# Kernel optimization log

Hardware: AMD Instinct MI355X
Metric: run time of the kernel (lower is better)

Reference implementation:

```python
import jax, jax.numpy as jnp
import numpy as np

N = 50000
E = 800000
F_IN = 128
HID = 32
HEADS = 4
SLOPE = 0.2


def setup_inputs() -> dict:
    key = jax.random.key(0)
    ks = jax.random.split(key, 12)
    x = jax.random.normal(ks[0], (N, F_IN), dtype=jnp.float32)
    edge_index = jax.random.randint(ks[1], (2, E), 0, N, dtype=jnp.int64)
    edge_attr = jax.random.normal(ks[2], (E, 4), dtype=jnp.float32)
    s1 = 1.0 / np.sqrt(F_IN)
    s2 = 1.0 / np.sqrt(HID)
    W1 = jax.random.normal(ks[3], (F_IN, HEADS * HID), dtype=jnp.float32) * s1
    a_src1 = jax.random.normal(ks[4], (HEADS, HID), dtype=jnp.float32) * s2
    a_dst1 = jax.random.normal(ks[5], (HEADS, HID), dtype=jnp.float32) * s2
    b1 = jnp.zeros((HID,), dtype=jnp.float32)
    W2 = jax.random.normal(ks[6], (HID, 1), dtype=jnp.float32) * s2
    a_src2 = jax.random.normal(ks[7], (1, 1), dtype=jnp.float32)
    a_dst2 = jax.random.normal(ks[8], (1, 1), dtype=jnp.float32)
    b2 = jnp.zeros((1,), dtype=jnp.float32)
    return {"input_tensor": x, "edge_index": edge_index, "edge_attr": edge_attr,
            "W1": W1, "a_src1": a_src1, "a_dst1": a_dst1, "b1": b1,
            "W2": W2, "a_src2": a_src2, "a_dst2": a_dst2, "b2": b2}


def _gat_conv(x, src, dst, W, a_src, a_dst, b, heads, out_ch):
    n = x.shape[0]
    h = (x @ W).reshape(n, heads, out_ch)          # [N, H, C]
    alpha_src = jnp.sum(h * a_src, axis=-1)        # [N, H]
    alpha_dst = jnp.sum(h * a_dst, axis=-1)        # [N, H]
    e = alpha_src[src] + alpha_dst[dst]            # [E, H]
    e = jax.nn.leaky_relu(e, negative_slope=SLOPE)
    # segment softmax over edges grouped by destination node
    e_max = jax.ops.segment_max(e, dst, num_segments=n)
    e = jnp.exp(e - e_max[dst])
    denom = jax.ops.segment_sum(e, dst, num_segments=n)
    alpha = e / denom[dst]                         # [E, H]
    msg = h[src] * alpha[..., None]                # [E, H, C]
    out = jax.ops.segment_sum(msg, dst, num_segments=n)  # [N, H, C]
    return out.mean(axis=1) + b                    # concat=False -> mean over heads


def reference(input_tensor, edge_index, edge_attr, W1, a_src1, a_dst1, b1, W2, a_src2, a_dst2, b2):
    # PyG GATConv adds self-loops by default; edge_attr unused (edge_dim=None)
    loops = jnp.arange(N, dtype=edge_index.dtype)
    src = jnp.concatenate([edge_index[0], loops])
    dst = jnp.concatenate([edge_index[1], loops])
    x = _gat_conv(input_tensor, src, dst, W1, a_src1, a_dst1, b1, HEADS, HID)
    x = jax.nn.elu(x)
    x = _gat_conv(x, src, dst, W2, a_src2, a_dst2, b2, 1, 1)
    return x
```

## Files before the change

kernel.cpp:

```cpp
#include <hip/hip_runtime.h>
#include <hip/hip_fp16.h>
#include <math.h>
#include <stdint.h>

static constexpr int kN     = 50000;
static constexpr int kFIn   = 128;
static constexpr int kHeads = 4;
static constexpr int kScanB = 256;
static constexpr int kScanNB = (kN + kScanB - 1) / kScanB;

typedef _Float16 half8v  __attribute__((ext_vector_type(8)));
typedef float    floatx4 __attribute__((ext_vector_type(4)));

__device__ __forceinline__ float lrelu(float x) { return x > 0.f ? x : 0.2f * x; }

__device__ __forceinline__ float pack2h(float a, float b) {
    const __half2 h = __floats2half2_rn(a, b);
    return __uint_as_float(__builtin_bit_cast(uint32_t, h));
}

__global__ void k_init(int* __restrict__ p, int n) {
    int i = blockIdx.x * blockDim.x + threadIdx.x;
    if (i < n) p[i] = 0;
}

__global__ __launch_bounds__(256)
void k_gemm1(const float* __restrict__ x, const float* __restrict__ W1,
             __half* __restrict__ h1h, int nPass, int grid) {
    __shared__ __align__(16) float whf[128 * 16 * 4];
    __shared__ __align__(16) float xsf[32 * 16 * 4];
    const int t = threadIdx.x;
    const int l = t & 63;
    const int g = t >> 6;
    for (int idx = t; idx < 2048; idx += 256) {
        const int c = idx >> 7, col = idx & 127;
        float4 st;
        st.x = pack2h(W1[(8 * c + 0) * 128 + col], W1[(8 * c + 1) * 128 + col]);
        st.y = pack2h(W1[(8 * c + 2) * 128 + col], W1[(8 * c + 3) * 128 + col]);
        st.z = pack2h(W1[(8 * c + 4) * 128 + col], W1[(8 * c + 5) * 128 + col]);
        st.w = pack2h(W1[(8 * c + 6) * 128 + col], W1[(8 * c + 7) * 128 + col]);
        const int gran = col * 16 + ((c + col) & 15);
        *reinterpret_cast<float4*>(&whf[gran * 4]) = st;
    }
    __syncthreads();

    const int rt  = g & 1;
    const int ctB = (g >> 1) * 4;
    const int lm  = l & 15;
    const int lk  = l >> 4;

    for (int pass = blockIdx.x; pass < nPass; pass += grid) {
        const int nodeBase = pass * 32;
        for (int q = t; q < 512; q += 256) {
            const int nn = q >> 4, ck = q & 15;
            int n = nodeBase + nn; if (n >= kN) n = kN - 1;
            const float4 xa = *reinterpret_cast<const float4*>(&x[(size_t)n * 128 + ck * 8]);
            const float4 xb = *reinterpret_cast<const float4*>(&x[(size_t)n * 128 + ck * 8 + 4]);
            float4 st;
            st.x = pack2h(xa.x, xa.y);
            st.y = pack2h(xa.z, xa.w);
            st.z = pack2h(xb.x, xb.y);
            st.w = pack2h(xb.z, xb.w);
            const int gran = nn * 16 + ((ck + nn) & 15);
            *reinterpret_cast<float4*>(&xsf[gran * 4]) = st;
        }
        __syncthreads();

        floatx4 acc0 = {0.f, 0.f, 0.f, 0.f};
        floatx4 acc1 = {0.f, 0.f, 0.f, 0.f};
        floatx4 acc2 = {0.f, 0.f, 0.f, 0.f};
        floatx4 acc3 = {0.f, 0.f, 0.f, 0.f};
        const int node = rt * 16 + lm;
        const int ch0  = ctB * 16 + lm;
#pragma unroll
        for (int kk = 0; kk < 4; ++kk) {
            const int ck = lk + 4 * kk;
            const half8v af = *reinterpret_cast<const half8v*>(
                &xsf[(node * 16 + ((ck + node) & 15)) * 4]);
            const half8v b0 = *reinterpret_cast<const half8v*>(
                &whf[((ch0 +  0) * 16 + ((ck + ch0 +  0) & 15)) * 4]);
            const half8v b1 = *reinterpret_cast<const half8v*>(
                &whf[((ch0 + 16) * 16 + ((ck + ch0 + 16) & 15)) * 4]);
            const half8v b2 = *reinterpret_cast<const half8v*>(
                &whf[((ch0 + 32) * 16 + ((ck + ch0 + 32) & 15)) * 4]);
            const half8v b3 = *reinterpret_cast<const half8v*>(
                &whf[((ch0 + 48) * 16 + ((ck + ch0 + 48) & 15)) * 4]);
            acc0 = __builtin_amdgcn_mfma_f32_16x16x32_f16(af, b0, acc0, 0, 0, 0);
            acc1 = __builtin_amdgcn_mfma_f32_16x16x32_f16(af, b1, acc1, 0, 0, 0);
            acc2 = __builtin_amdgcn_mfma_f32_16x16x32_f16(af, b2, acc2, 0, 0, 0);
            acc3 = __builtin_amdgcn_mfma_f32_16x16x32_f16(af, b3, acc3, 0, 0, 0);
        }
        const int nrow0 = nodeBase + rt * 16 + lk * 4;
#pragma unroll
        for (int r = 0; r < 4; ++r) {
            const int n = nrow0 + r;
            if (n < kN) {
                h1h[(size_t)n * 128 + ch0     ] = __float2half(acc0[r]);
                h1h[(size_t)n * 128 + ch0 + 16] = __float2half(acc1[r]);
                h1h[(size_t)n * 128 + ch0 + 32] = __float2half(acc2[r]);
                h1h[(size_t)n * 128 + ch0 + 48] = __float2half(acc3[r]);
            }
        }
        __syncthreads();
    }
}

__global__ __launch_bounds__(256)
void k_logits(const __half* __restrict__ h1h,
              const float* __restrict__ a_src1, const float* __restrict__ a_dst1,
              float* __restrict__ asrc, float* __restrict__ adst) {
    const int n = blockIdx.x * 4 + (threadIdx.x >> 6);
    if (n >= kN) return;
    const int j = threadIdx.x & 63;
    const float2 f = __half22float2(*(const __half2*)&h1h[(size_t)n * 128 + 2 * j]);
    float ps = f.x * a_src1[2 * j] + f.y * a_src1[2 * j + 1];
    float pd = f.x * a_dst1[2 * j] + f.y * a_dst1[2 * j + 1];
#pragma unroll
    for (int off = 8; off >= 1; off >>= 1) {
        ps += __shfl_xor(ps, off, 64);
        pd += __shfl_xor(pd, off, 64);
    }
    if ((j & 15) == 0) {
        asrc[n * 4 + (j >> 4)] = ps;
        adst[n * 4 + (j >> 4)] = pd;
    }
}

__global__ void k_hist(const int* __restrict__ ei, int E, int* __restrict__ deg,
                       int* __restrict__ rank) {
    int i = blockIdx.x * blockDim.x + threadIdx.x;
    int total = E + kN;
    if (i >= total) return;
    int d = (i < E) ? ei[E + i] : (i - E);
    rank[i] = atomicAdd(&deg[d], 1);
}

__global__ void k_scan_a(const int* __restrict__ deg, int* __restrict__ loc, int* __restrict__ bsum) {
    __shared__ int tmp[kScanB];
    int t = threadIdx.x;
    int i = blockIdx.x * kScanB + t;
    int v = (i < kN) ? deg[i] : 0;
    tmp[t] = v;
    __syncthreads();
    for (int off = 1; off < kScanB; off <<= 1) {
        int add = (t >= off) ? tmp[t - off] : 0;
        __syncthreads();
        tmp[t] += add;
        __syncthreads();
    }
    if (i < kN) loc[i] = tmp[t] - v;
    if (t == kScanB - 1) bsum[blockIdx.x] = tmp[t];
}

__global__ void k_scan_b(int* __restrict__ bsum) {
    __shared__ int tmp[256];
    int t = threadIdx.x;
    int v = (t < kScanNB) ? bsum[t] : 0;
    tmp[t] = v;
    __syncthreads();
    for (int off = 1; off < 256; off <<= 1) {
        int add = (t >= off) ? tmp[t - off] : 0;
        __syncthreads();
        tmp[t] += add;
        __syncthreads();
    }
    if (t < kScanNB) bsum[t] = tmp[t] - v;
}

__global__ void k_scan_c(const int* __restrict__ loc, const int* __restrict__ bsum,
                         int* __restrict__ rowptr, int E2) {
    int i = blockIdx.x * kScanB + threadIdx.x;
    if (i < kN) rowptr[i] = loc[i] + bsum[blockIdx.x];
    if (i == 0) rowptr[kN] = E2;
}

__global__ void k_scatter(const int* __restrict__ ei, int E,
                          const int* __restrict__ rowptr, const int* __restrict__ rank,
                          int* __restrict__ es) {
    int i = blockIdx.x * blockDim.x + threadIdx.x;
    int total = E + kN;
    if (i >= total) return;
    int s, d;
    if (i < E) { s = ei[i]; d = ei[E + i]; } else { s = d = i - E; }
    es[rowptr[d] + rank[i]] = s;
}

__global__ __launch_bounds__(256)
void k_wgt(const int* __restrict__ rowptr, const int* __restrict__ es,
           const float* __restrict__ asrc, const float* __restrict__ adst,
           float* __restrict__ wgt) {
    const int n = blockIdx.x * 16 + (threadIdx.x >> 4);
    if (n >= kN) return;
    const int l = threadIdx.x & 15;
    const int beg = rowptr[n], end = rowptr[n + 1];
    const float ad0 = adst[n * 4 + 0], ad1 = adst[n * 4 + 1];
    const float ad2 = adst[n * 4 + 2], ad3 = adst[n * 4 + 3];
    for (int p = beg + l; p < end; p += 16) {
        const int s = es[p];
        float4 w4;
        w4.x = expf(lrelu(asrc[s * 4 + 0] + ad0));
        w4.y = expf(lrelu(asrc[s * 4 + 1] + ad1));
        w4.z = expf(lrelu(asrc[s * 4 + 2] + ad2));
        w4.w = expf(lrelu(asrc[s * 4 + 3] + ad3));
        *reinterpret_cast<float4*>(&wgt[(size_t)p * 4]) = w4;
    }
}

__global__ __launch_bounds__(256)
void k_agg1(const int* __restrict__ rowptr, const int* __restrict__ es,
            const float* __restrict__ wgt,
            const __half* __restrict__ h1h, const float* __restrict__ b1,
            const float* __restrict__ W2, float* __restrict__ h2) {
    const int n = blockIdx.x * 4 + (threadIdx.x >> 6);
    if (n >= kN) return;
    const int j  = threadIdx.x & 63;
    const int hh = j >> 4;
    const int beg = rowptr[n], end = rowptr[n + 1];
    float ax0 = 0.f, ay0 = 0.f, dn0 = 0.f;
    float ax1 = 0.f, ay1 = 0.f, dn1 = 0.f;
    int p = beg;
    for (; p + 4 <= end; p += 4) {
        const int s0 = es[p],     s1 = es[p + 1];
        const int s2 = es[p + 2], s3 = es[p + 3];
        const float w0 = wgt[(p + 0) * 4 + hh];
        const float w1 = wgt[(p + 1) * 4 + hh];
        const float w2 = wgt[(p + 2) * 4 + hh];
        const float w3 = wgt[(p + 3) * 4 + hh];
        const float2 f0 = __half22float2(*(const __half2*)&h1h[s0 * 128 + 2 * j]);
        const float2 f1 = __half22float2(*(const __half2*)&h1h[s1 * 128 + 2 * j]);
        const float2 f2 = __half22float2(*(const __half2*)&h1h[s2 * 128 + 2 * j]);
        const float2 f3 = __half22float2(*(const __half2*)&h1h[s3 * 128 + 2 * j]);
        ax0 += w0 * f0.x; ay0 += w0 * f0.y; dn0 += w0;
        ax1 += w1 * f1.x; ay1 += w1 * f1.y; dn1 += w1;
        ax0 += w2 * f2.x; ay0 += w2 * f2.y; dn0 += w2;
        ax1 += w3 * f3.x; ay1 += w3 * f3.y; dn1 += w3;
    }
    for (; p < end; ++p) {
        const int s0 = es[p];
        const float w0 = wgt[p * 4 + hh];
        const float2 f0 = __half22float2(*(const __half2*)&h1h[s0 * 128 + 2 * j]);
        ax0 += w0 * f0.x; ay0 += w0 * f0.y; dn0 += w0;
    }
    const float den = dn0 + dn1;
    float vx = (ax0 + ax1) / den;
    float vy = (ay0 + ay1) / den;
    vx += __shfl_xor(vx, 32, 64); vy += __shfl_xor(vy, 32, 64);
    vx += __shfl_xor(vx, 16, 64); vy += __shfl_xor(vy, 16, 64);
    const int m = j & 15;
    float u0 = 0.25f * vx + b1[2 * m];
    float u1 = 0.25f * vy + b1[2 * m + 1];
    u0 = u0 > 0.f ? u0 : expf(u0) - 1.f;
    u1 = u1 > 0.f ? u1 : expf(u1) - 1.f;
    float tsum = u0 * W2[2 * m] + u1 * W2[2 * m + 1];
    tsum += __shfl_xor(tsum, 8, 64);
    tsum += __shfl_xor(tsum, 4, 64);
    tsum += __shfl_xor(tsum, 2, 64);
    tsum += __shfl_xor(tsum, 1, 64);
    if (j == 0) h2[n] = tsum;
}

__global__ __launch_bounds__(256)
void k_agg2(const int* __restrict__ rowptr, const int* __restrict__ es,
            const float* __restrict__ h2,
            const float* __restrict__ a_s2, const float* __restrict__ a_d2,
            const float* __restrict__ b2, float* __restrict__ out) {
    const int n = blockIdx.x * 16 + (threadIdx.x >> 4);
    if (n >= kN) return;
    const int l = threadIdx.x & 15;
    const float as = a_s2[0], ad = a_d2[0];
    const int beg = rowptr[n], end = rowptr[n + 1];
    const float hd = h2[n] * ad;
    float sw = 0.f, swh = 0.f;
    for (int p = beg + l; p < end; p += 16) {
        float hs = h2[es[p]];
        float w = expf(lrelu(hs * as + hd));
        sw += w;
        swh += w * hs;
    }
#pragma unroll
    for (int off = 8; off >= 1; off >>= 1) {
        sw  += __shfl_xor(sw, off, 64);
        swh += __shfl_xor(swh, off, 64);
    }
    if (l == 0) out[n] = swh / sw + b2[0];
}

extern "C" void kernel_launch(void* const* d_in, const int* in_sizes, int n_in,
                              void* d_out, int out_size, void* d_ws, size_t ws_size,
                              hipStream_t stream) {
    const float* x      = (const float*)d_in[0];
    const int*   ei     = (const int*)d_in[1];
    const float* W1     = (const float*)d_in[3];
    const float* a_src1 = (const float*)d_in[4];
    const float* a_dst1 = (const float*)d_in[5];
    const float* b1     = (const float*)d_in[6];
    const float* W2     = (const float*)d_in[7];
    const float* a_src2 = (const float*)d_in[8];
    const float* a_dst2 = (const float*)d_in[9];
    const float* b2     = (const float*)d_in[10];
    float* out = (float*)d_out;

    const int E  = in_sizes[1] / 2;
    const int E2 = E + kN;

    float*  ws    = (float*)d_ws;
    float*  asrc  = ws;
    float*  adst  = ws + 200000;
    float*  h2    = ws + 400000;
    __half* h1h   = (__half*)(ws + 450000);
    float*  wgt   = ws + 3650000;
    int*    ibase = (int*)(ws + 7050000);
    int*    es     = ibase;
    int*    deg    = ibase + 850000;
    int*    rank   = ibase + 900000;
    int*    loc    = ibase + 1750000;
    int*    rowptr = ibase + 1800000;
    int*    bsum   = ibase + 1850016;

    k_init<<<(kN + 255) / 256, 256, 0, stream>>>(deg, kN);

    k_hist<<<(E2 + 255) / 256, 256, 0, stream>>>(ei, E, deg, rank);
    k_scan_a<<<kScanNB, kScanB, 0, stream>>>(deg, loc, bsum);
    k_scan_b<<<1, 256, 0, stream>>>(bsum);
    k_scan_c<<<kScanNB, kScanB, 0, stream>>>(loc, bsum, rowptr, E2);

    {
        const int nPass = (kN + 31) / 32;
        const int grid  = 782;
        k_gemm1<<<grid, 256, 0, stream>>>(x, W1, h1h, nPass, grid);
    }

    k_logits<<<(kN + 3) / 4, 256, 0, stream>>>(h1h, a_src1, a_dst1, asrc, adst);

    k_scatter<<<(E2 + 255) / 256, 256, 0, stream>>>(ei, E, rowptr, rank, es);

    k_wgt<<<(kN + 15) / 16, 256, 0, stream>>>(rowptr, es, asrc, adst, wgt);

    k_agg1<<<(kN + 3) / 4, 256, 0, stream>>>(rowptr, es, wgt, h1h, b1, W2, h2);

    k_agg2<<<(kN + 15) / 16, 256, 0, stream>>>(rowptr, es, h2, a_src2, a_dst2, b2, out);
}
```

Measured before the change: 145.6 us.

## Normalize attention weights in k_wgt, store fp16 alpha, accumulate in half2

k_wgt now computes the per-destination softmax denominator itself, using a two-pass loop and a 16-lane shuffle reduction. It then writes normalized attention coefficients as fp16 instead of raw fp32 exp weights. k_agg1 reads half-size alpha values and accumulates messages with packed half2 FMAs, with no per-edge denominator tracking and no final division. This halves the weight traffic and cuts ALU work in the aggregation. In exchange it recomputes the exps twice in k_wgt and accumulates in fp16, which risks precision loss on high-degree nodes.

```diff
diff --git a/kernel.cpp b/kernel.cpp
--- a/kernel.cpp
+++ b/kernel.cpp
@@ -188,27 +188,45 @@
 __global__ __launch_bounds__(256)
 void k_wgt(const int* __restrict__ rowptr, const int* __restrict__ es,
            const float* __restrict__ asrc, const float* __restrict__ adst,
-           float* __restrict__ wgt) {
+           __half* __restrict__ alphaH) {
     const int n = blockIdx.x * 16 + (threadIdx.x >> 4);
     if (n >= kN) return;
     const int l = threadIdx.x & 15;
     const int beg = rowptr[n], end = rowptr[n + 1];
     const float ad0 = adst[n * 4 + 0], ad1 = adst[n * 4 + 1];
     const float ad2 = adst[n * 4 + 2], ad3 = adst[n * 4 + 3];
+    float t0 = 0.f, t1 = 0.f, t2 = 0.f, t3 = 0.f;
     for (int p = beg + l; p < end; p += 16) {
         const int s = es[p];
-        float4 w4;
-        w4.x = expf(lrelu(asrc[s * 4 + 0] + ad0));
-        w4.y = expf(lrelu(asrc[s * 4 + 1] + ad1));
-        w4.z = expf(lrelu(asrc[s * 4 + 2] + ad2));
-        w4.w = expf(lrelu(asrc[s * 4 + 3] + ad3));
-        *reinterpret_cast<float4*>(&wgt[(size_t)p * 4]) = w4;
+        t0 += expf(lrelu(asrc[s * 4 + 0] + ad0));
+        t1 += expf(lrelu(asrc[s * 4 + 1] + ad1));
+        t2 += expf(lrelu(asrc[s * 4 + 2] + ad2));
+        t3 += expf(lrelu(asrc[s * 4 + 3] + ad3));
+    }
+#pragma unroll
+    for (int off = 8; off >= 1; off >>= 1) {
+        t0 += __shfl_xor(t0, off, 64);
+        t1 += __shfl_xor(t1, off, 64);
+        t2 += __shfl_xor(t2, off, 64);
+        t3 += __shfl_xor(t3, off, 64);
+    }
+    const float r0 = 1.f / t0, r1 = 1.f / t1, r2 = 1.f / t2, r3 = 1.f / t3;
+    for (int p = beg + l; p < end; p += 16) {
+        const int s = es[p];
+        const float w0 = expf(lrelu(asrc[s * 4 + 0] + ad0)) * r0;
+        const float w1 = expf(lrelu(asrc[s * 4 + 1] + ad1)) * r1;
+        const float w2 = expf(lrelu(asrc[s * 4 + 2] + ad2)) * r2;
+        const float w3 = expf(lrelu(asrc[s * 4 + 3] + ad3)) * r3;
+        float2 st;
+        st.x = pack2h(w0, w1);
+        st.y = pack2h(w2, w3);
+        *reinterpret_cast<float2*>(&alphaH[(size_t)p * 4]) = st;
     }
 }
 
 __global__ __launch_bounds__(256)
 void k_agg1(const int* __restrict__ rowptr, const int* __restrict__ es,
-            const float* __restrict__ wgt,
+            const __half* __restrict__ alphaH,
             const __half* __restrict__ h1h, const float* __restrict__ b1,
             const float* __restrict__ W2, float* __restrict__ h2) {
     const int n = blockIdx.x * 4 + (threadIdx.x >> 6);
@@ -216,34 +234,35 @@
     const int j  = threadIdx.x & 63;
     const int hh = j >> 4;
     const int beg = rowptr[n], end = rowptr[n + 1];
-    float ax0 = 0.f, ay0 = 0.f, dn0 = 0.f;
-    float ax1 = 0.f, ay1 = 0.f, dn1 = 0.f;
+    const __half2* h12 = (const __half2*)h1h;
+    __half2 accA = __floats2half2_rn(0.f, 0.f);
+    __half2 accB = __floats2half2_rn(0.f, 0.f);
     int p = beg;
     for (; p + 4 <= end; p += 4) {
         const int s0 = es[p],     s1 = es[p + 1];
         const int s2 = es[p + 2], s3 = es[p + 3];
-        const float w0 = wgt[(p + 0) * 4 + hh];
-        const float w1 = wgt[(p + 1) * 4 + hh];
-        const float w2 = wgt[(p + 2) * 4 + hh];
-        const float w3 = wgt[(p + 3) * 4 + hh];
-        const float2 f0 = __half22float2(*(const __half2*)&h1h[s0 * 128 + 2 * j]);
-        const float2 f1 = __half22float2(*(const __half2*)&h1h[s1 * 128 + 2 * j]);
-        const float2 f2 = __half22float2(*(const __half2*)&h1h[s2 * 128 + 2 * j]);
-        const float2 f3 = __half22float2(*(const __half2*)&h1h[s3 * 128 + 2 * j]);
-        ax0 += w0 * f0.x; ay0 += w0 * f0.y; dn0 += w0;
-        ax1 += w1 * f1.x; ay1 += w1 * f1.y; dn1 += w1;
-        ax0 += w2 * f2.x; ay0 += w2 * f2.y; dn0 += w2;
-        ax1 += w3 * f3.x; ay1 += w3 * f3.y; dn1 += w3;
+        const __half a0 = alphaH[(size_t)(p + 0) * 4 + hh];
+        const __half a1 = alphaH[(size_t)(p + 1) * 4 + hh];
+        const __half a2 = alphaH[(size_t)(p + 2) * 4 + hh];
+        const __half a3 = alphaH[(size_t)(p + 3) * 4 + hh];
+        const __half2 v0 = h12[(size_t)s0 * 64 + j];
+        const __half2 v1 = h12[(size_t)s1 * 64 + j];
+        const __half2 v2 = h12[(size_t)s2 * 64 + j];
+        const __half2 v3 = h12[(size_t)s3 * 64 + j];
+        accA = __hfma2(__half2half2(a0), v0, accA);
+        accB = __hfma2(__half2half2(a1), v1, accB);
+        accA = __hfma2(__half2half2(a2), v2, accA);
+        accB = __hfma2(__half2half2(a3), v3, accB);
     }
     for (; p < end; ++p) {
         const int s0 = es[p];
-        const float w0 = wgt[p * 4 + hh];
-        const float2 f0 = __half22float2(*(const __half2*)&h1h[s0 * 128 + 2 * j]);
-        ax0 += w0 * f0.x; ay0 += w0 * f0.y; dn0 += w0;
-    }
-    const float den = dn0 + dn1;
-    float vx = (ax0 + ax1) / den;
-    float vy = (ay0 + ay1) / den;
+        const __half a0 = alphaH[(size_t)p * 4 + hh];
+        accA = __hfma2(__half2half2(a0), h12[(size_t)s0 * 64 + j], accA);
+    }
+    const float2 fa = __half22float2(accA);
+    const float2 fb = __half22float2(accB);
+    float vx = fa.x + fb.x;
+    float vy = fa.y + fb.y;
     vx += __shfl_xor(vx, 32, 64); vy += __shfl_xor(vy, 32, 64);
     vx += __shfl_xor(vx, 16, 64); vy += __shfl_xor(vy, 16, 64);
     const int m = j & 15;
@@ -308,8 +327,8 @@
     float*  adst  = ws + 200000;
     float*  h2    = ws + 400000;
     __half* h1h   = (__half*)(ws + 450000);
-    float*  wgt   = ws + 3650000;
-    int*    ibase = (int*)(ws + 7050000);
+    __half* alphaH= (__half*)(ws + 3650000);
+    int*    ibase = (int*)(ws + 5350000);
     int*    es     = ibase;
     int*    deg    = ibase + 850000;
     int*    rank   = ibase + 900000;
@@ -334,9 +353,9 @@
 
     k_scatter<<<(E2 + 255) / 256, 256, 0, stream>>>(ei, E, rowptr, rank, es);
 
-    k_wgt<<<(kN + 15) / 16, 256, 0, stream>>>(rowptr, es, asrc, adst, wgt);
-
-    k_agg1<<<(kN + 3) / 4, 256, 0, stream>>>(rowptr, es, wgt, h1h, b1, W2, h2);
+    k_wgt<<<(kN + 15) / 16, 256, 0, stream>>>(rowptr, es, asrc, adst, alphaH);
+
+    k_agg1<<<(kN + 3) / 4, 256, 0, stream>>>(rowptr, es, alphaH, h1h, b1, W2, h2);
 
     k_agg2<<<(kN + 15) / 16, 256, 0, stream>>>(rowptr, es, h2, a_src2, a_dst2, b2, out);
 }
```

Result: no change. 147.5 us (+1.3%).
